# Kernel tuning notes

Hardware: AMD Instinct MI355X
Metric: run time of the kernel (lower is better)

## Reference

```python
import jax, jax.numpy as jnp
import numpy as np


def setup_inputs() -> dict:
    key = jax.random.key(0)
    k1, k2, k3, k4 = jax.random.split(key, 4)
    B, C, H, W = 16, 64, 128, 128
    x = jax.random.normal(k1, (B, C, H, W), dtype=jnp.float32)
    y = jax.random.normal(k2, (B, C, H, W), dtype=jnp.float32)
    # nn.Parameter(torch.zeros(1)) in the original; use small random values so
    # the attention branch contributes (zeros would make it a pure residual).
    temperature1 = jax.random.normal(k3, (1,), dtype=jnp.float32) * 0.1
    temperature2 = jax.random.normal(k4, (1,), dtype=jnp.float32) * 0.1
    return {"x": x, "y": y, "temperature1": temperature1,
            "temperature2": temperature2, "num_heads": 4}


def _l2norm_lastdim(v):
    # F.normalize(v, dim=-1): v / max(||v||_2, eps)
    n = jnp.sqrt(jnp.sum(v * v, axis=-1, keepdims=True))
    return v / jnp.maximum(n, 1e-12)


def reference(x, y, temperature1, temperature2, num_heads):
    B, C, H, W = x.shape
    c = C // num_heads
    HW = H * W
    # b (head c) h w -> b head c (h w)
    xr = x.reshape(B, num_heads, c, HW)
    yr = y.reshape(B, num_heads, c, HW)

    # key_x normalized over (h w); key_y (b head (hw) c) normalized over dim=-2,
    # which is the same (h w) axis of yr in 'bhck' layout.
    key_x = _l2norm_lastdim(xr)
    key_y = _l2norm_lastdim(yr)
    # energy[b,h,c,d] = sum_k key_x[b,h,c,k] * key_y[b,h,d,k]  -> (B, head, c, c)
    energy = jnp.einsum('bhck,bhdk->bhcd', key_x, key_y)

    attn1 = jax.nn.softmax(energy, axis=-1)                        # (B,h,c,c)
    attn2 = jax.nn.softmax(energy.transpose(0, 1, 3, 2), axis=-1)  # (B,h,c,c)

    # y_att (b head (hw) c) = value_y @ attn1, then 'b head (h w) c -> b (head c) h w'
    # out[b,h,d,k] = sum_c attn1[b,h,c,d] * yr[b,h,c,k]
    y_att = jnp.einsum('bhcd,bhck->bhdk', attn1, yr).reshape(B, C, H, W)
    x_att = jnp.einsum('bhcd,bhck->bhdk', attn2, xr).reshape(B, C, H, W)

    y_ = temperature1[0] * y_att + x
    x_ = temperature2[0] * x_att + y
    return jnp.concatenate((x_, y_), axis=1)  # (B, 2C, H, W)
```

## Files before the change

kernel.cpp:

```cpp
#include <hip/hip_runtime.h>

#define HW      16384
#define CPH     16
#define NBH     64
#define NSLICE  16
#define KSLICE  (HW / NSLICE)
#define TKT     256
#define LS      260
#define KPT     4
#define PSTRIDE 288


__global__ __launch_bounds__(256) void gram_kernel(
    const float* __restrict__ x,
    const float* __restrict__ y,
    float* __restrict__ ws)
{
    __shared__ float xs[16 * LS];
    __shared__ float ys[16 * LS];
    __shared__ float Gs[256];
    __shared__ float sxs[16], sys[16];

    const int blk  = blockIdx.x;
    const int bh   = blk >> 4;
    const int sl   = blk & 15;
    const int ks   = sl * KSLICE;
    const int t    = threadIdx.x;

    Gs[t] = 0.f;
    if (t < 16) { sxs[t] = 0.f; sys[t] = 0.f; }

    const int c0 = t & 3;
    const int d0 = (t >> 2) & 3;
    const int g  = t >> 4;

    const int srow = t >> 6;
    const int scol = (t & 63) * 4;

    float acc[4][4];
    #pragma unroll
    for (int i = 0; i < 4; ++i)
        #pragma unroll
        for (int j = 0; j < 4; ++j) acc[i][j] = 0.f;
    float sqx[4] = {0.f, 0.f, 0.f, 0.f};
    float sqy[4] = {0.f, 0.f, 0.f, 0.f};

    const float* xb = x + (size_t)bh * CPH * HW + ks;
    const float* yb = y + (size_t)bh * CPH * HW + ks;

    float4 px[4], py[4];
    #pragma unroll
    for (int i = 0; i < 4; ++i) {
        const size_t off = (size_t)(i * 4 + srow) * HW + scol;
        px[i] = *reinterpret_cast<const float4*>(xb + off);
        py[i] = *reinterpret_cast<const float4*>(yb + off);
    }

    for (int kt = 0; kt < KSLICE; kt += TKT) {
        __syncthreads();
        #pragma unroll
        for (int i = 0; i < 4; ++i) {
            *reinterpret_cast<float4*>(&xs[(i * 4 + srow) * LS + scol]) = px[i];
            *reinterpret_cast<float4*>(&ys[(i * 4 + srow) * LS + scol]) = py[i];
        }
        __syncthreads();

        if (kt + TKT < KSLICE) {
            #pragma unroll
            for (int i = 0; i < 4; ++i) {
                const size_t off = (size_t)(i * 4 + srow) * HW + (kt + TKT) + scol;
                px[i] = *reinterpret_cast<const float4*>(xb + off);
                py[i] = *reinterpret_cast<const float4*>(yb + off);
            }
        }

        #pragma unroll
        for (int kq = 0; kq < 16; kq += 4) {
            float4 xr[4], yr[4];
            #pragma unroll
            for (int i = 0; i < 4; ++i)
                xr[i] = *reinterpret_cast<const float4*>(&xs[(c0 + 4 * i) * LS + g * 16 + kq]);
            #pragma unroll
            for (int j = 0; j < 4; ++j)
                yr[j] = *reinterpret_cast<const float4*>(&ys[(d0 + 4 * j) * LS + g * 16 + kq]);
            #pragma unroll
            for (int i = 0; i < 4; ++i)
                #pragma unroll
                for (int j = 0; j < 4; ++j) {
                    acc[i][j] = fmaf(xr[i].x, yr[j].x, acc[i][j]);
                    acc[i][j] = fmaf(xr[i].y, yr[j].y, acc[i][j]);
                    acc[i][j] = fmaf(xr[i].z, yr[j].z, acc[i][j]);
                    acc[i][j] = fmaf(xr[i].w, yr[j].w, acc[i][j]);
                }
            if (d0 == 0) {
                #pragma unroll
                for (int i = 0; i < 4; ++i) {
                    sqx[i] = fmaf(xr[i].x, xr[i].x, sqx[i]);
                    sqx[i] = fmaf(xr[i].y, xr[i].y, sqx[i]);
                    sqx[i] = fmaf(xr[i].z, xr[i].z, sqx[i]);
                    sqx[i] = fmaf(xr[i].w, xr[i].w, sqx[i]);
                }
            }
            if (c0 == 0) {
                #pragma unroll
                for (int j = 0; j < 4; ++j) {
                    sqy[j] = fmaf(yr[j].x, yr[j].x, sqy[j]);
                    sqy[j] = fmaf(yr[j].y, yr[j].y, sqy[j]);
                    sqy[j] = fmaf(yr[j].z, yr[j].z, sqy[j]);
                    sqy[j] = fmaf(yr[j].w, yr[j].w, sqy[j]);
                }
            }
        }
    }

    #pragma unroll
    for (int i = 0; i < 4; ++i)
        #pragma unroll
        for (int j = 0; j < 4; ++j)
            atomicAdd(&Gs[(c0 + 4 * i) * 16 + (d0 + 4 * j)], acc[i][j]);
    if (d0 == 0) {
        #pragma unroll
        for (int i = 0; i < 4; ++i) atomicAdd(&sxs[c0 + 4 * i], sqx[i]);
    }
    if (c0 == 0) {
        #pragma unroll
        for (int j = 0; j < 4; ++j) atomicAdd(&sys[d0 + 4 * j], sqy[j]);
    }
    __syncthreads();

    float* P = ws + (size_t)(bh * NSLICE + sl) * PSTRIDE;
    P[t] = Gs[t];
    if (t < 16)       P[256 + t] = sxs[t];
    else if (t < 32)  P[272 + (t - 16)] = sys[t - 16];
}

__global__ __launch_bounds__(256) void apply_kernel(
    const float* __restrict__ x,
    const float* __restrict__ y,
    const float* __restrict__ ws,
    const float* __restrict__ t1p,
    const float* __restrict__ t2p,
    float* __restrict__ out)
{
    const int CHUNKS = HW / (256 * KPT);
    const int blk   = blockIdx.x;
    const int bh    = blk / CHUNKS;
    const int chunk = blk % CHUNKS;
    const int t     = threadIdx.x;
    const int k0    = chunk * (256 * KPT) + t * KPT;
    const int i     = t >> 4;
    const int j     = t & 15;

    __shared__ float  Es[256];
    __shared__ float2 Ws[256];
    __shared__ float  nxs[16], nys[16];

    const float* P = ws + (size_t)bh * NSLICE * PSTRIDE;
    float gsum = 0.f;
    #pragma unroll
    for (int s = 0; s < NSLICE; ++s) gsum += P[s * PSTRIDE + t];
    if (t < 32) {
        const int off = (t < 16) ? (256 + t) : (272 + (t - 16));
        float q = 0.f;
        #pragma unroll
        for (int s = 0; s < NSLICE; ++s) q += P[s * PSTRIDE + off];
        float n = fmaxf(sqrtf(q), 1e-12f);
        if (t < 16) nxs[t] = n; else nys[t - 16] = n;
    }
    __syncthreads();

    const float e = gsum / (nxs[i] * nys[j]);
    Es[t] = e;
    __syncthreads();

    float rm = -1e30f;
    #pragma unroll
    for (int r = 0; r < 16; ++r) rm = fmaxf(rm, Es[i * 16 + r]);
    float rs = 0.f;
    #pragma unroll
    for (int r = 0; r < 16; ++r) rs += expf(Es[i * 16 + r] - rm);
    const float a1 = expf(e - rm) / rs;

    float cm = -1e30f;
    #pragma unroll
    for (int r = 0; r < 16; ++r) cm = fmaxf(cm, Es[r * 16 + j]);
    float cs = 0.f;
    #pragma unroll
    for (int r = 0; r < 16; ++r) cs += expf(Es[r * 16 + j] - cm);
    const float v2 = expf(e - cm) / cs;

    const float t1 = t1p[0];
    const float t2 = t2p[0];
    float* Wsf = reinterpret_cast<float*>(Ws);
    Wsf[(i * 16 + j) * 2 + 1] = t1 * a1;
    Wsf[(j * 16 + i) * 2 + 0] = t2 * v2;
    __syncthreads();

    const int b = bh >> 2;
    const int h = bh & 3;

    const float* xbase = x + ((size_t)bh * CPH) * HW + k0;
    const float* ybase = y + ((size_t)bh * CPH) * HW + k0;

    float accx[16][KPT];
    float accy[16][KPT];
    #pragma unroll
    for (int d = 0; d < 16; ++d)
        #pragma unroll
        for (int q = 0; q < KPT; ++q) { accx[d][q] = 0.f; accy[d][q] = 0.f; }

    float4 xq[2], yq[2];
    xq[0] = *reinterpret_cast<const float4*>(xbase);
    yq[0] = *reinterpret_cast<const float4*>(ybase);
    xq[1] = *reinterpret_cast<const float4*>(xbase + (size_t)1 * HW);
    yq[1] = *reinterpret_cast<const float4*>(ybase + (size_t)1 * HW);

    #pragma unroll
    for (int c = 0; c < 16; ++c) {
        const float4 xv = xq[c & 1];
        const float4 yv = yq[c & 1];
        if (c + 2 < 16) {
            xq[c & 1] = *reinterpret_cast<const float4*>(xbase + (size_t)(c + 2) * HW);
            yq[c & 1] = *reinterpret_cast<const float4*>(ybase + (size_t)(c + 2) * HW);
        }
        #pragma unroll
        for (int d = 0; d < 16; ++d) {
            float2 w = Ws[c * 16 + d];
            accx[d][0] = fmaf(w.x, xv.x, accx[d][0]);
            accx[d][1] = fmaf(w.x, xv.y, accx[d][1]);
            accx[d][2] = fmaf(w.x, xv.z, accx[d][2]);
            accx[d][3] = fmaf(w.x, xv.w, accx[d][3]);
            accy[d][0] = fmaf(w.y, yv.x, accy[d][0]);
            accy[d][1] = fmaf(w.y, yv.y, accy[d][1]);
            accy[d][2] = fmaf(w.y, yv.z, accy[d][2]);
            accy[d][3] = fmaf(w.y, yv.w, accy[d][3]);
        }
        accx[c][0] += yv.x;  accx[c][1] += yv.y;  accx[c][2] += yv.z;  accx[c][3] += yv.w;
        accy[c][0] += xv.x;  accy[c][1] += xv.y;  accy[c][2] += xv.z;  accy[c][3] += xv.w;
    }

    const size_t obx = ((size_t)b * 128 + h * 16) * HW + k0;
    const size_t oby = obx + (size_t)64 * HW;
    #pragma unroll
    for (int d = 0; d < 16; ++d) {
        float4 px = make_float4(accx[d][0], accx[d][1], accx[d][2], accx[d][3]);
        float4 py = make_float4(accy[d][0], accy[d][1], accy[d][2], accy[d][3]);
        *reinterpret_cast<float4*>(out + obx + (size_t)d * HW) = px;
        *reinterpret_cast<float4*>(out + oby + (size_t)d * HW) = py;
    }
}

extern "C" void kernel_launch(void* const* d_in, const int* in_sizes, int n_in,
                              void* d_out, int out_size, void* d_ws, size_t ws_size,
                              hipStream_t stream) {
    const float* x  = (const float*)d_in[0];
    const float* y  = (const float*)d_in[1];
    const float* t1 = (const float*)d_in[2];
    const float* t2 = (const float*)d_in[3];
    float* ws  = (float*)d_ws;
    float* out = (float*)d_out;

    gram_kernel<<<NBH * NSLICE, 256, 0, stream>>>(x, y, ws);
    apply_kernel<<<NBH * (HW / (256 * KPT)), 256, 0, stream>>>(x, y, ws, t1, t2, out);
}
```

Baseline: 317.9 us.

## Rewrite gram kernel with register-tiled 8x8 per-wave blocks and shuffle reduction

The gram kernel drops its shared-memory staging and LDS atomics. Each wave now owns an 8x8 block of the 16x16 Gram matrix and reads its x/y rows straight from global memory into registers. A butterfly shuffle-transpose reduction across lanes finishes the sums, and the slice count drops from 16 to 8, so fewer partials are written. This removes LDS traffic and barriers, but each x/y row is read by two waves, uses 64 accumulators per thread, and loses the explicit prefetch double-buffering.

```diff
diff --git a/kernel.cpp b/kernel.cpp
--- a/kernel.cpp
+++ b/kernel.cpp
@@ -3,10 +3,8 @@
 #define HW      16384
 #define CPH     16
 #define NBH     64
-#define NSLICE  16
-#define KSLICE  (HW / NSLICE)
-#define TKT     256
-#define LS      260
+#define NSLICE  8
+#define KBLK    (HW / NSLICE)
 #define KPT     4
 #define PSTRIDE 288
 
@@ -16,122 +14,88 @@
     const float* __restrict__ y,
     float* __restrict__ ws)
 {
-    __shared__ float xs[16 * LS];
-    __shared__ float ys[16 * LS];
-    __shared__ float Gs[256];
-    __shared__ float sxs[16], sys[16];
-
     const int blk  = blockIdx.x;
-    const int bh   = blk >> 4;
-    const int sl   = blk & 15;
-    const int ks   = sl * KSLICE;
+    const int bh   = blk >> 3;
+    const int kb   = blk & 7;
     const int t    = threadIdx.x;
-
-    Gs[t] = 0.f;
-    if (t < 16) { sxs[t] = 0.f; sys[t] = 0.f; }
-
-    const int c0 = t & 3;
-    const int d0 = (t >> 2) & 3;
-    const int g  = t >> 4;
-
-    const int srow = t >> 6;
-    const int scol = (t & 63) * 4;
-
-    float acc[4][4];
-    #pragma unroll
-    for (int i = 0; i < 4; ++i)
-        #pragma unroll
-        for (int j = 0; j < 4; ++j) acc[i][j] = 0.f;
-    float sqx[4] = {0.f, 0.f, 0.f, 0.f};
-    float sqy[4] = {0.f, 0.f, 0.f, 0.f};
-
-    const float* xb = x + (size_t)bh * CPH * HW + ks;
-    const float* yb = y + (size_t)bh * CPH * HW + ks;
-
-    float4 px[4], py[4];
-    #pragma unroll
-    for (int i = 0; i < 4; ++i) {
-        const size_t off = (size_t)(i * 4 + srow) * HW + scol;
-        px[i] = *reinterpret_cast<const float4*>(xb + off);
-        py[i] = *reinterpret_cast<const float4*>(yb + off);
-    }
-
-    for (int kt = 0; kt < KSLICE; kt += TKT) {
-        __syncthreads();
-        #pragma unroll
-        for (int i = 0; i < 4; ++i) {
-            *reinterpret_cast<float4*>(&xs[(i * 4 + srow) * LS + scol]) = px[i];
-            *reinterpret_cast<float4*>(&ys[(i * 4 + srow) * LS + scol]) = py[i];
-        }
-        __syncthreads();
-
-        if (kt + TKT < KSLICE) {
+    const int w    = t >> 6;
+    const int lane = t & 63;
+    const int cq   = (w >> 1) * 8;
+    const int dq   = (w & 1) * 8;
+
+    const float* xb = x + (size_t)bh * CPH * HW + (size_t)cq * HW
+                        + (size_t)kb * KBLK + (size_t)lane * 4;
+    const float* yb = y + (size_t)bh * CPH * HW + (size_t)dq * HW
+                        + (size_t)kb * KBLK + (size_t)lane * 4;
+
+    float acc[64];
+    #pragma unroll
+    for (int v = 0; v < 64; ++v) acc[v] = 0.f;
+    float sq[8] = {0.f, 0.f, 0.f, 0.f, 0.f, 0.f, 0.f, 0.f};
+    const bool sq_is_x = (w == 0) || (w == 3);
+
+    for (int it = 0; it < KBLK; it += 256) {
+        float4 xr[8], yr[8];
+        #pragma unroll
+        for (int i = 0; i < 8; ++i) {
+            xr[i] = *reinterpret_cast<const float4*>(xb + (size_t)i * HW + it);
+            yr[i] = *reinterpret_cast<const float4*>(yb + (size_t)i * HW + it);
+        }
+        #pragma unroll
+        for (int i = 0; i < 8; ++i)
             #pragma unroll
-            for (int i = 0; i < 4; ++i) {
-                const size_t off = (size_t)(i * 4 + srow) * HW + (kt + TKT) + scol;
-                px[i] = *reinterpret_cast<const float4*>(xb + off);
-                py[i] = *reinterpret_cast<const float4*>(yb + off);
+            for (int j = 0; j < 8; ++j) {
+                float a = acc[i * 8 + j];
+                a = fmaf(xr[i].x, yr[j].x, a);
+                a = fmaf(xr[i].y, yr[j].y, a);
+                a = fmaf(xr[i].z, yr[j].z, a);
+                a = fmaf(xr[i].w, yr[j].w, a);
+                acc[i * 8 + j] = a;
             }
-        }
-
-        #pragma unroll
-        for (int kq = 0; kq < 16; kq += 4) {
-            float4 xr[4], yr[4];
-            #pragma unroll
-            for (int i = 0; i < 4; ++i)
-                xr[i] = *reinterpret_cast<const float4*>(&xs[(c0 + 4 * i) * LS + g * 16 + kq]);
-            #pragma unroll
-            for (int j = 0; j < 4; ++j)
-                yr[j] = *reinterpret_cast<const float4*>(&ys[(d0 + 4 * j) * LS + g * 16 + kq]);
-            #pragma unroll
-            for (int i = 0; i < 4; ++i)
-                #pragma unroll
-                for (int j = 0; j < 4; ++j) {
-                    acc[i][j] = fmaf(xr[i].x, yr[j].x, acc[i][j]);
-                    acc[i][j] = fmaf(xr[i].y, yr[j].y, acc[i][j]);
-                    acc[i][j] = fmaf(xr[i].z, yr[j].z, acc[i][j]);
-                    acc[i][j] = fmaf(xr[i].w, yr[j].w, acc[i][j]);
-                }
-            if (d0 == 0) {
-                #pragma unroll
-                for (int i = 0; i < 4; ++i) {
-                    sqx[i] = fmaf(xr[i].x, xr[i].x, sqx[i]);
-                    sqx[i] = fmaf(xr[i].y, xr[i].y, sqx[i]);
-                    sqx[i] = fmaf(xr[i].z, xr[i].z, sqx[i]);
-                    sqx[i] = fmaf(xr[i].w, xr[i].w, sqx[i]);
-                }
-            }
-            if (c0 == 0) {
-                #pragma unroll
-                for (int j = 0; j < 4; ++j) {
-                    sqy[j] = fmaf(yr[j].x, yr[j].x, sqy[j]);
-                    sqy[j] = fmaf(yr[j].y, yr[j].y, sqy[j]);
-                    sqy[j] = fmaf(yr[j].z, yr[j].z, sqy[j]);
-                    sqy[j] = fmaf(yr[j].w, yr[j].w, sqy[j]);
-                }
-            }
-        }
-    }
-
-    #pragma unroll
-    for (int i = 0; i < 4; ++i)
-        #pragma unroll
-        for (int j = 0; j < 4; ++j)
-            atomicAdd(&Gs[(c0 + 4 * i) * 16 + (d0 + 4 * j)], acc[i][j]);
-    if (d0 == 0) {
-        #pragma unroll
-        for (int i = 0; i < 4; ++i) atomicAdd(&sxs[c0 + 4 * i], sqx[i]);
-    }
-    if (c0 == 0) {
-        #pragma unroll
-        for (int j = 0; j < 4; ++j) atomicAdd(&sys[d0 + 4 * j], sqy[j]);
-    }
-    __syncthreads();
-
-    float* P = ws + (size_t)(bh * NSLICE + sl) * PSTRIDE;
-    P[t] = Gs[t];
-    if (t < 16)       P[256 + t] = sxs[t];
-    else if (t < 32)  P[272 + (t - 16)] = sys[t - 16];
+        #pragma unroll
+        for (int i = 0; i < 8; ++i) {
+            const float4 v = sq_is_x ? xr[i] : yr[i];
+            sq[i] = fmaf(v.x, v.x, sq[i]);
+            sq[i] = fmaf(v.y, v.y, sq[i]);
+            sq[i] = fmaf(v.z, v.z, sq[i]);
+            sq[i] = fmaf(v.w, v.w, sq[i]);
+        }
+    }
+
+    #pragma unroll
+    for (int s = 0; s < 6; ++s) {
+        const int m    = 1 << s;
+        const int K    = 64 >> s;
+        const int keep = (lane >> s) & 1;
+        #pragma unroll
+        for (int idx = 0; idx < K; idx += 2) {
+            const float a = acc[idx]     + __shfl_xor(acc[idx],     m, 64);
+            const float b = acc[idx + 1] + __shfl_xor(acc[idx + 1], m, 64);
+            acc[idx >> 1] = keep ? b : a;
+        }
+    }
+    #pragma unroll
+    for (int s = 0; s < 3; ++s) {
+        const int m    = 1 << s;
+        const int K    = 8 >> s;
+        const int keep = (lane >> s) & 1;
+        #pragma unroll
+        for (int idx = 0; idx < K; idx += 2) {
+            const float a = sq[idx]     + __shfl_xor(sq[idx],     m, 64);
+            const float b = sq[idx + 1] + __shfl_xor(sq[idx + 1], m, 64);
+            sq[idx >> 1] = keep ? b : a;
+        }
+    }
+    sq[0] += __shfl_xor(sq[0],  8, 64);
+    sq[0] += __shfl_xor(sq[0], 16, 64);
+    sq[0] += __shfl_xor(sq[0], 32, 64);
+
+    float* P = ws + (size_t)(bh * NSLICE + kb) * PSTRIDE;
+    P[(cq + (lane >> 3)) * 16 + (dq + (lane & 7))] = acc[0];
+    if (lane < 8) {
+        if (sq_is_x) P[256 + cq + lane] = sq[0];
+        else         P[272 + dq + lane] = sq[0];
+    }
 }
 
 __global__ __launch_bounds__(256) void apply_kernel(
```

New measurement: 275.5 us. 1.15x faster.
